# Performance work log

Hardware: AMD Instinct MI355X
Metric: run time of the kernel (lower is better)

Reference implementation:

```python
import jax, jax.numpy as jnp
import numpy as np

B, C, H, W = 8, 128, 96, 96
E = 8           # num_experts
K = 3           # active_experts
HID = 4 * C     # hidden dim of each expert (hidden_ratio=4)


def _conv1x1(x, w, b):
    # x: [B,C,H,W], w: [O,C], b: [O] -> [B,O,H,W]
    return jnp.einsum('bchw,oc->bohw', x, w) + b[None, :, None, None]


def setup_inputs() -> dict:
    key = jax.random.key(0)
    ks = jax.random.split(key, 12)
    s = lambda k, shape, fan_in: jax.random.normal(k, shape, jnp.float32) * (1.0 / np.sqrt(fan_in))
    return {
        'x':   jax.random.normal(ks[0], (B, C, H, W), jnp.float32),
        # shared expert: Conv2d(C->HID,1x1), GELU, Conv2d(HID->C,1x1)
        'sw1': s(ks[1], (HID, C), C),   'sb1': jnp.zeros((HID,), jnp.float32),
        'sw2': s(ks[2], (C, HID), HID), 'sb2': jnp.zeros((C,), jnp.float32),
        # router gate: Conv2d(C->E,1x1)
        'gw':  s(ks[3], (E, C), C),     'gb':  jnp.zeros((E,), jnp.float32),
        # stacked routed experts
        'ew1': s(ks[4], (E, HID, C), C),   'eb1': jnp.zeros((E, HID), jnp.float32),
        'ew2': s(ks[5], (E, C, HID), HID), 'eb2': jnp.zeros((E, C), jnp.float32),
    }


def reference(x, sw1, sb1, sw2, sb2, gw, gb, ew1, eb1, ew2, eb2):
    # shared expert (exact GELU, matching torch nn.GELU default)
    h_s = jax.nn.gelu(_conv1x1(x, sw1, sb1), approximate=False)
    shared_out = _conv1x1(h_s, sw2, sb2)

    # router: softmax over expert dim, top-k, renormalize
    logits = _conv1x1(x, gw, gb)                      # [B,E,H,W]
    scores = jax.nn.softmax(logits, axis=1)           # [B,E,H,W]
    s_last = jnp.transpose(scores, (0, 2, 3, 1))      # [B,H,W,E]
    topk_probs, topk_idx = jax.lax.top_k(s_last, K)   # [B,H,W,K]
    topk_probs = topk_probs / jnp.sum(topk_probs, axis=-1, keepdims=True)

    # expert_mask[b,e,h,w]: routing weight for expert e at location (scatter-equivalent)
    onehot = jax.nn.one_hot(topk_idx, E, dtype=x.dtype)        # [B,H,W,K,E]
    mask = jnp.einsum('bhwke,bhwk->behw', onehot, topk_probs)  # [B,E,H,W]

    # dense compute of all experts (faithful to original), masked combine
    h = jax.nn.gelu(jnp.einsum('bchw,eoc->beohw', x, ew1)
                    + eb1[None, :, :, None, None], approximate=False)  # [B,E,HID,H,W]
    y = jnp.einsum('beohw,eco->bechw', h, ew2) + eb2[None, :, :, None, None]
    moe_out = jnp.einsum('bechw,behw->bchw', y, mask)

    # load-balancing aux loss
    mean_prob = jnp.mean(scores, axis=(0, 2, 3))               # [E]
    mean_load = jnp.mean(jnp.sum(onehot, axis=3), axis=(0, 1, 2))  # [E]
    aux_loss = E * jnp.sum(mean_prob * mean_load)

    return (x + shared_out + moe_out, aux_loss)
```

## Files before the change

### kernel.cpp

```cpp
#include <hip/hip_runtime.h>


typedef __bf16 bf16x8 __attribute__((ext_vector_type(8)));
typedef __bf16 bf16x2 __attribute__((ext_vector_type(2)));
typedef unsigned short u16x8 __attribute__((ext_vector_type(8)));
typedef float f32x4 __attribute__((ext_vector_type(4)));

#define HWP 9216
#define NPIX 73728
#define LDX 136
#define LDH 136
#define LXP 68
#define MAXSLOTS 77312
#define MAXTILES 1208
#define NSH 16

__device__ __forceinline__ unsigned short f2bf(float f) {
    return __builtin_bit_cast(unsigned short, (__bf16)f);
}

__device__ __forceinline__ unsigned pk_bf16(float a, float b) {
    bf16x2 v; v[0] = (__bf16)a; v[1] = (__bf16)b;
    return __builtin_bit_cast(unsigned, v);
}

__device__ __forceinline__ float bf2f(unsigned short h) {
    return __uint_as_float((unsigned)h << 16);
}

__device__ __forceinline__ float fast_gelu(float x) {
    float x2 = x * x;
    float u = x * fmaf(0.0356774081f, x2, 0.7978845608f);
    float e = __builtin_amdgcn_exp2f(u * 2.8853900818f);
    float r = __builtin_amdgcn_rcpf(e + 1.0f);
    float t = fmaf(-2.0f, r, 1.0f);
    float s = 0.5f * x;
    return fmaf(s, t, s);
}

__device__ __forceinline__ f32x4 mfma16(u16x8 a, u16x8 b, f32x4 c) {
    return __builtin_amdgcn_mfma_f32_16x16x32_bf16(
        __builtin_bit_cast(bf16x8, a), __builtin_bit_cast(bf16x8, b), c, 0, 0, 0);
}

__global__ __launch_bounds__(256) void router_fused(
    const float* __restrict__ x, const float* __restrict__ gw,
    const float* __restrict__ gb,
    const float* __restrict__ sw1, const float* __restrict__ sw2,
    const float* __restrict__ ew1, const float* __restrict__ ew2,
    unsigned short* __restrict__ wbf,
    unsigned short* __restrict__ xT,
    int* __restrict__ pixmask, float* __restrict__ pixw3,
    int* __restrict__ pixaux,
    int* __restrict__ bincount, float* __restrict__ accum)
{
    __shared__ float gws[1024];
    __shared__ float xls[128 * LXP];
    __shared__ float part[4 * 64 * 8];

    const int tid = threadIdx.x;
    const int blk = blockIdx.x;
    const int shadow = blk & (NSH - 1);

    {
        int i = blk * 256 + tid;
        #pragma unroll
        for (int j = 0; j < 4; ++j) {
            float v;
            if (i < 65536) v = sw1[i];
            else if (i < 131072) v = sw2[i - 65536];
            else if (i < 655360) v = ew1[i - 131072];
            else v = ew2[i - 655360];
            wbf[i] = f2bf(v);
            i += 1152 * 256;
        }
    }

    for (int i = tid; i < 1024; i += 256) gws[i] = gw[i];

    const int b = blk / 144;
    const int p0 = (blk - b * 144) * 64;
    const float* xb = x + (size_t)b * 128 * HWP + p0;

    #pragma unroll
    for (int j = 0; j < 8; ++j) {
        int id4 = j * 256 + tid;
        int c = id4 >> 4;
        int g = id4 & 15;
        f32x4 v = *(const f32x4*)(xb + (size_t)c * HWP + g * 4);
        *(f32x4*)&xls[c * LXP + g * 4] = v;
    }
    __syncthreads();

    const int p = tid & 63, q = tid >> 6;
    {
        float lg[8];
        #pragma unroll
        for (int e = 0; e < 8; ++e) lg[e] = 0.f;
        #pragma unroll
        for (int k = 0; k < 32; ++k) {
            int c = q * 32 + k;
            float xv = xls[c * LXP + p];
            #pragma unroll
            for (int e = 0; e < 8; ++e) lg[e] = fmaf(xv, gws[e * 128 + c], lg[e]);
        }
        #pragma unroll
        for (int e = 0; e < 8; ++e) part[(q * 64 + p) * 8 + e] = lg[e];
    }
    __syncthreads();

    if (tid < 64) {
        const int gp = b * HWP + p0 + tid;
        float l2[8];
        #pragma unroll
        for (int e = 0; e < 8; ++e)
            l2[e] = gb[e] + part[tid * 8 + e] + part[(64 + tid) * 8 + e]
                  + part[(128 + tid) * 8 + e] + part[(192 + tid) * 8 + e];
        float mx = l2[0];
        #pragma unroll
        for (int e = 1; e < 8; ++e) mx = fmaxf(mx, l2[e]);
        float pr[8]; float s = 0.f;
        #pragma unroll
        for (int e = 0; e < 8; ++e) { pr[e] = __expf(l2[e] - mx); s += pr[e]; }
        float sinv = __builtin_amdgcn_rcpf(s);
        #pragma unroll
        for (int e = 0; e < 8; ++e) pr[e] *= sinv;

        unsigned chosen = 0; float topsum = 0.f;
        for (int k = 0; k < 3; ++k) {
            int best = 0; float bv = -1.f;
            #pragma unroll
            for (int e = 0; e < 8; ++e) {
                bool ok = !((chosen >> e) & 1u) && pr[e] > bv;
                bv = ok ? pr[e] : bv;
                best = ok ? e : best;
            }
            chosen |= 1u << best;
            topsum += bv;
        }
        float tinv = __builtin_amdgcn_rcpf(topsum);

        pixmask[gp] = (int)chosen;
        {
            int j = 0;
            #pragma unroll
            for (int e = 0; e < 8; ++e)
                if ((chosen >> e) & 1u) { pixw3[gp * 3 + j] = pr[e] * tinv; ++j; }
        }

        unsigned long long eq = ~0ull;
        #pragma unroll
        for (int bit = 0; bit < 8; ++bit) {
            unsigned long long bb = __ballot((chosen >> bit) & 1u);
            eq &= ((chosen >> bit) & 1u) ? bb : ~bb;
        }
        const unsigned long long lowmask = (tid == 0) ? 0ull : (~0ull >> (64 - tid));
        int rank = __popcll(eq & lowmask);
        int cnt = __popcll(eq);
        int leader = __ffsll((unsigned long long)eq) - 1;
        int off_val = 0;
        if (rank == 0) off_val = atomicAdd(&bincount[shadow * 256 + (int)chosen], cnt);
        int binoff = __shfl(off_val, leader);
        pixaux[gp] = binoff + rank;

        #pragma unroll
        for (int e = 0; e < 8; ++e) {
            float v = pr[e];
            float c2 = ((chosen >> e) & 1u) ? 1.f : 0.f;
            #pragma unroll
            for (int off = 32; off > 0; off >>= 1) {
                v += __shfl_down(v, off);
                c2 += __shfl_down(c2, off);
            }
            if (tid == 0) {
                atomicAdd(&accum[shadow * 16 + e], v);
                atomicAdd(&accum[shadow * 16 + 8 + e], c2);
            }
        }
    }

    {
        const int pp = tid >> 2, qq = tid & 3;
        unsigned short* dst = xT + ((size_t)(blk * 64 + pp)) * 128 + qq * 32;
        #pragma unroll
        for (int j = 0; j < 4; ++j) {
            const int c0 = qq * 32 + j * 8;
            uint4 wv;
            wv.x = pk_bf16(xls[(c0 + 0) * LXP + pp], xls[(c0 + 1) * LXP + pp]);
            wv.y = pk_bf16(xls[(c0 + 2) * LXP + pp], xls[(c0 + 3) * LXP + pp]);
            wv.z = pk_bf16(xls[(c0 + 4) * LXP + pp], xls[(c0 + 5) * LXP + pp]);
            wv.w = pk_bf16(xls[(c0 + 6) * LXP + pp], xls[(c0 + 7) * LXP + pp]);
            *(uint4*)(dst + j * 8) = wv;
        }
    }
}

__global__ __launch_bounds__(256) void fill_bins(
    const int* __restrict__ bincount, const int* __restrict__ pixmask,
    int* __restrict__ idx, int* __restrict__ pixaux,
    int* __restrict__ tileMask, int* __restrict__ tileBase,
    int* __restrict__ ntiles)
{
    __shared__ int spc[256], snt[256], bb[256];
    __shared__ int sbase[NSH][256];
    const int tid = threadIdx.x;
    int c = 0;
    #pragma unroll
    for (int s = 0; s < NSH; ++s) {
        sbase[s][tid] = c;
        c += bincount[s * 256 + tid];
    }
    const int nt = (c + 63) >> 6;
    const int pc = nt << 6;
    spc[tid] = pc; snt[tid] = nt;
    __syncthreads();
    #pragma unroll
    for (int off = 1; off < 256; off <<= 1) {
        int a = (tid >= off) ? spc[tid - off] : 0;
        int d = (tid >= off) ? snt[tid - off] : 0;
        __syncthreads();
        spc[tid] += a; snt[tid] += d;
        __syncthreads();
    }
    const int base = spc[tid] - pc;
    bb[tid] = base;
    if (blockIdx.x == 0) {
        const int tstart = snt[tid] - nt;
        for (int j = 0; j < nt; ++j) {
            tileMask[tstart + j] = tid;
            tileBase[tstart + j] = base + (j << 6);
        }
        if (tid == 255) ntiles[0] = snt[255];
    }
    __syncthreads();

    const int gp = blockIdx.x * 256 + tid;
    int mask = pixmask[gp];
    int shadow = (gp >> 6) & (NSH - 1);
    int slot = bb[mask] + sbase[shadow][mask] + pixaux[gp];
    idx[slot] = gp;
    pixaux[gp] = slot;
}

__global__ __launch_bounds__(256, 3) void moe_sparse(
    const unsigned short* __restrict__ xT, const int* __restrict__ idx,
    const float* __restrict__ pixw3,
    const int* __restrict__ tileMask, const int* __restrict__ tileBase,
    const int* __restrict__ ntiles,
    const unsigned short* __restrict__ wbf,
    const float* __restrict__ sb1, const float* __restrict__ sb2,
    const float* __restrict__ eb1, const float* __restrict__ eb2,
    unsigned short* __restrict__ outT)
{
    __shared__ unsigned short xs[64 * LDX];
    __shared__ unsigned short hs[64 * LDH];
    __shared__ float wls[64 * 4];

    const int t = blockIdx.x;
    if (t >= ntiles[0]) return;
    const int mask = tileMask[t];
    const int base = tileBase[t];
    const int tid = threadIdx.x;

    {
        const int p = tid >> 2, q = tid & 3;
        const int gp = idx[base + p];
        const unsigned short* src = xT + (size_t)gp * 128 + q * 32;
        unsigned short* dst = &xs[p * LDX + q * 32];
        #pragma unroll
        for (int j = 0; j < 4; ++j)
            *(u16x8*)(dst + j * 8) = *(const u16x8*)(src + j * 8);
        if (q == 0) {
            wls[p * 4 + 0] = pixw3[gp * 3 + 0];
            wls[p * 4 + 1] = pixw3[gp * 3 + 1];
            wls[p * 4 + 2] = pixw3[gp * 3 + 2];
        }
    }
    __syncthreads();

    int el[3];
    { int n = 0;
      #pragma unroll
      for (int e = 0; e < 8; ++e) if ((mask >> e) & 1) { if (n < 3) el[n] = e; ++n; } }

    const int wave = tid >> 6;
    const int lr = tid & 15;
    const int lq = (tid >> 4) & 3;

    const f32x4 vzero = {0.f, 0.f, 0.f, 0.f};
    f32x4 fin[2][4];
    #pragma unroll
    for (int t2 = 0; t2 < 2; ++t2)
        #pragma unroll
        for (int nt2 = 0; nt2 < 4; ++nt2) fin[t2][nt2] = vzero;

    for (int pass = 0; pass < 4; ++pass) {
        const unsigned short* w1; const unsigned short* w2;
        const float* b1;
        if (pass == 0) { w1 = wbf; b1 = sb1; w2 = wbf + 65536; }
        else {
            int e = el[pass - 1];
            w1 = wbf + 131072 + (size_t)e * (512 * 128);  b1 = eb1 + e * 512;
            w2 = wbf + 655360 + (size_t)e * (128 * 512);
        }

        float wtv[4];
        #pragma unroll
        for (int nt2 = 0; nt2 < 4; ++nt2)
            wtv[nt2] = (pass == 0) ? 1.0f : wls[(nt2 * 16 + lr) * 4 + (pass - 1)];

        for (int chunk = 0; chunk < 4; ++chunk) {
            u16x8 w1f[2][4];
            #pragma unroll
            for (int t2 = 0; t2 < 2; ++t2) {
                const int hid0 = chunk * 128 + wave * 32 + t2 * 16;
                const u16x8* wr = (const u16x8*)(w1 + (size_t)(hid0 + lr) * 128) + lq;
                #pragma unroll
                for (int ks = 0; ks < 4; ++ks) w1f[t2][ks] = wr[ks * 4];
            }
            f32x4 acc[2][4];
            #pragma unroll
            for (int t2 = 0; t2 < 2; ++t2)
                #pragma unroll
                for (int nt2 = 0; nt2 < 4; ++nt2) acc[t2][nt2] = vzero;
            __builtin_amdgcn_s_setprio(1);
            #pragma unroll
            for (int ks = 0; ks < 4; ++ks) {
                #pragma unroll
                for (int nt2 = 0; nt2 < 4; ++nt2) {
                    u16x8 xf = *(const u16x8*)&xs[(nt2 * 16 + lr) * LDX + ks * 32 + lq * 8];
                    acc[0][nt2] = mfma16(w1f[0][ks], xf, acc[0][nt2]);
                    acc[1][nt2] = mfma16(w1f[1][ks], xf, acc[1][nt2]);
                }
            }
            __builtin_amdgcn_s_setprio(0);

            u16x8 w2f[2][4];
            #pragma unroll
            for (int t2 = 0; t2 < 2; ++t2) {
                const int c0 = wave * 32 + t2 * 16;
                const u16x8* wr = (const u16x8*)(w2 + (size_t)(c0 + lr) * 512 + chunk * 128) + lq;
                #pragma unroll
                for (int ks = 0; ks < 4; ++ks) w2f[t2][ks] = wr[ks * 4];
            }

            #pragma unroll
            for (int t2 = 0; t2 < 2; ++t2) {
                const int hl = wave * 32 + t2 * 16 + lq * 4;
                const f32x4 b1v = *(const f32x4*)&b1[chunk * 128 + hl];
                #pragma unroll
                for (int nt2 = 0; nt2 < 4; ++nt2) {
                    float g0 = wtv[nt2] * fast_gelu(acc[t2][nt2][0] + b1v[0]);
                    float g1 = wtv[nt2] * fast_gelu(acc[t2][nt2][1] + b1v[1]);
                    float g2 = wtv[nt2] * fast_gelu(acc[t2][nt2][2] + b1v[2]);
                    float g3 = wtv[nt2] * fast_gelu(acc[t2][nt2][3] + b1v[3]);
                    uint2 wv = {pk_bf16(g0, g1), pk_bf16(g2, g3)};
                    *(uint2*)&hs[(nt2 * 16 + lr) * LDH + hl] = wv;
                }
            }
            __syncthreads();
            __builtin_amdgcn_s_setprio(1);
            #pragma unroll
            for (int ks = 0; ks < 4; ++ks) {
                #pragma unroll
                for (int nt2 = 0; nt2 < 4; ++nt2) {
                    u16x8 hb = *(const u16x8*)&hs[(nt2 * 16 + lr) * LDH + ks * 32 + lq * 8];
                    fin[0][nt2] = mfma16(w2f[0][ks], hb, fin[0][nt2]);
                    fin[1][nt2] = mfma16(w2f[1][ks], hb, fin[1][nt2]);
                }
            }
            __builtin_amdgcn_s_setprio(0);
            __syncthreads();
        }
    }

    #pragma unroll
    for (int t2 = 0; t2 < 2; ++t2) {
        const int cidx = wave * 32 + t2 * 16 + lq * 4;
        const f32x4 s2v = *(const f32x4*)&sb2[cidx];
        const f32x4 e0v = *(const f32x4*)&eb2[el[0] * 128 + cidx];
        const f32x4 e1v = *(const f32x4*)&eb2[el[1] * 128 + cidx];
        const f32x4 e2v = *(const f32x4*)&eb2[el[2] * 128 + cidx];
        #pragma unroll
        for (int nt2 = 0; nt2 < 4; ++nt2) {
            const float w0 = wls[(nt2 * 16 + lr) * 4 + 0];
            const float w1 = wls[(nt2 * 16 + lr) * 4 + 1];
            const float w2 = wls[(nt2 * 16 + lr) * 4 + 2];
            float o[4];
            #pragma unroll
            for (int r = 0; r < 4; ++r) {
                float bsum = s2v[r];
                bsum = fmaf(w0, e0v[r], bsum);
                bsum = fmaf(w1, e1v[r], bsum);
                bsum = fmaf(w2, e2v[r], bsum);
                o[r] = fin[t2][nt2][r] + bsum;
            }
            unsigned short* dst = outT + ((size_t)(base + nt2 * 16 + lr)) * 128
                                + wave * 32 + t2 * 16 + lq * 4;
            uint2 wv = {pk_bf16(o[0], o[1]), pk_bf16(o[2], o[3])};
            *(uint2*)dst = wv;
        }
    }
}

__global__ __launch_bounds__(256) void final_add(
    const float* __restrict__ x, const unsigned short* __restrict__ outT,
    const int* __restrict__ pixslot, const float* __restrict__ accum,
    float* __restrict__ out)
{
    if (blockIdx.x == 0 && threadIdx.x == 0) {
        float a16[16];
        #pragma unroll
        for (int i = 0; i < 16; ++i) {
            float s = 0.f;
            #pragma unroll
            for (int sh = 0; sh < NSH; ++sh) s += accum[sh * 16 + i];
            a16[i] = s;
        }
        float aux = 0.f;
        #pragma unroll
        for (int e = 0; e < 8; ++e) aux += a16[e] * a16[8 + e];
        out[9437184] = 8.0f * aux / ((float)NPIX * (float)NPIX);
    }
    __shared__ unsigned short ts[64 * 133];
    const int blk = blockIdx.x;
    const int b = blk / 144;
    const int p0 = (blk - b * 144) * 64;
    const int tid = threadIdx.x;
    {
        const int p = tid >> 2, q = tid & 3;
        const int slot = pixslot[blk * 64 + p];
        const unsigned short* src = outT + (size_t)slot * 128 + q * 32;
        unsigned short* dst = &ts[p * 133 + q * 32];
        #pragma unroll
        for (int j = 0; j < 4; ++j)
            *(u16x8*)(dst + j * 8) = *(const u16x8*)(src + j * 8);
    }
    __syncthreads();
    const int pl = tid & 63, cq = tid >> 6;
    const float* xb = x + (size_t)b * 128 * HWP + p0;
    float* ob = out + (size_t)b * 128 * HWP + p0;
    #pragma unroll
    for (int c0 = 0; c0 < 128; c0 += 4) {
        int c = c0 + cq;
        ob[(size_t)c * HWP + pl] = xb[(size_t)c * HWP + pl] + bf2f(ts[pl * 133 + c]);
    }
}

extern "C" void kernel_launch(void* const* d_in, const int* in_sizes, int n_in,
                              void* d_out, int out_size, void* d_ws, size_t ws_size,
                              hipStream_t stream)
{
    const float* x   = (const float*)d_in[0];
    const float* sw1 = (const float*)d_in[1];
    const float* sb1 = (const float*)d_in[2];
    const float* sw2 = (const float*)d_in[3];
    const float* sb2 = (const float*)d_in[4];
    const float* gw  = (const float*)d_in[5];
    const float* gb  = (const float*)d_in[6];
    const float* ew1 = (const float*)d_in[7];
    const float* eb1 = (const float*)d_in[8];
    const float* ew2 = (const float*)d_in[9];
    const float* eb2 = (const float*)d_in[10];
    float* out = (float*)d_out;
    char* ws = (char*)d_ws;

    const size_t o_wbf     = 0;
    const size_t o_xT      = 2359296;
    const size_t o_outT    = o_xT + 18874368;
    const size_t o_pixmask = o_outT + 19791872;
    const size_t o_pixw3   = o_pixmask + 294912;
    const size_t o_pixaux  = o_pixw3 + 884736;
    const size_t o_tmask   = o_pixaux + 294912;
    const size_t o_tbase   = o_tmask + 4864;
    const size_t o_idx     = o_tbase + 4864;
    const size_t o_cnt     = o_idx + 309248;
    const size_t o_ntiles  = o_cnt + 16384;
    const size_t o_accum   = o_ntiles + 16;
    const size_t MEMSET_SZ = 309248 + 16384 + 16 + 1024;

    unsigned short* wbf  = (unsigned short*)(ws + o_wbf);
    unsigned short* xT   = (unsigned short*)(ws + o_xT);
    unsigned short* outT = (unsigned short*)(ws + o_outT);
    int* pixmask  = (int*)(ws + o_pixmask);
    float* pixw3  = (float*)(ws + o_pixw3);
    int* pixaux   = (int*)(ws + o_pixaux);
    int* tmask    = (int*)(ws + o_tmask);
    int* tbase    = (int*)(ws + o_tbase);
    int* idx      = (int*)(ws + o_idx);
    int* bincount = (int*)(ws + o_cnt);
    int* ntiles   = (int*)(ws + o_ntiles);
    float* accum  = (float*)(ws + o_accum);

    (void)hipMemsetAsync(ws + o_idx, 0, MEMSET_SZ, stream);
    router_fused<<<1152, 256, 0, stream>>>(x, gw, gb, sw1, sw2, ew1, ew2, wbf,
                                           xT, pixmask, pixw3, pixaux, bincount, accum);
    fill_bins<<<288, 256, 0, stream>>>(bincount, pixmask, idx, pixaux,
                                       tmask, tbase, ntiles);
    moe_sparse<<<MAXTILES, 256, 0, stream>>>(xT, idx, pixw3, tmask, tbase, ntiles,
        wbf, sb1, sb2, eb1, eb2, outT);
    final_add<<<1152, 256, 0, stream>>>(x, outT, pixaux, accum, out);
}
```

Before: 321.6 us.

## Split moe_sparse work across 8 waves with 16-row slices per wave

Doubles the moe_sparse block from 4 to 8 waves. Each wave now owns 16 hidden/output rows instead of 32, which halves the per-wave accumulators and weight fragments. The x-tile load is spread over 512 threads. The aim is more resident waves to hide latency of global weight loads and LDS traffic, at the cost of each xs/hs fragment read being reused by only one MFMA instead of two, and more barrier participants.

```diff
diff --git a/kernel.cpp b/kernel.cpp
--- a/kernel.cpp
+++ b/kernel.cpp
@@ -242,7 +242,7 @@
     pixaux[gp] = slot;
 }
 
-__global__ __launch_bounds__(256, 3) void moe_sparse(
+__global__ __launch_bounds__(512, 6) void moe_sparse(
     const unsigned short* __restrict__ xT, const int* __restrict__ idx,
     const float* __restrict__ pixw3,
     const int* __restrict__ tileMask, const int* __restrict__ tileBase,
@@ -263,13 +263,12 @@
     const int tid = threadIdx.x;
 
     {
-        const int p = tid >> 2, q = tid & 3;
+        const int p = tid >> 3, q = tid & 7;
         const int gp = idx[base + p];
-        const unsigned short* src = xT + (size_t)gp * 128 + q * 32;
-        unsigned short* dst = &xs[p * LDX + q * 32];
-        #pragma unroll
-        for (int j = 0; j < 4; ++j)
-            *(u16x8*)(dst + j * 8) = *(const u16x8*)(src + j * 8);
+        const unsigned short* src = xT + (size_t)gp * 128 + q * 16;
+        unsigned short* dst = &xs[p * LDX + q * 16];
+        *(u16x8*)(dst + 0) = *(const u16x8*)(src + 0);
+        *(u16x8*)(dst + 8) = *(const u16x8*)(src + 8);
         if (q == 0) {
             wls[p * 4 + 0] = pixw3[gp * 3 + 0];
             wls[p * 4 + 1] = pixw3[gp * 3 + 1];
@@ -283,16 +282,14 @@
       #pragma unroll
       for (int e = 0; e < 8; ++e) if ((mask >> e) & 1) { if (n < 3) el[n] = e; ++n; } }
 
-    const int wave = tid >> 6;
+    const int w8 = tid >> 6;
     const int lr = tid & 15;
     const int lq = (tid >> 4) & 3;
 
     const f32x4 vzero = {0.f, 0.f, 0.f, 0.f};
-    f32x4 fin[2][4];
+    f32x4 fin[4];
     #pragma unroll
-    for (int t2 = 0; t2 < 2; ++t2)
-        #pragma unroll
-        for (int nt2 = 0; nt2 < 4; ++nt2) fin[t2][nt2] = vzero;
+    for (int nt2 = 0; nt2 < 4; ++nt2) fin[nt2] = vzero;
 
     for (int pass = 0; pass < 4; ++pass) {
         const unsigned short* w1; const unsigned short* w2;
@@ -310,50 +307,44 @@
             wtv[nt2] = (pass == 0) ? 1.0f : wls[(nt2 * 16 + lr) * 4 + (pass - 1)];
 
         for (int chunk = 0; chunk < 4; ++chunk) {
-            u16x8 w1f[2][4];
-            #pragma unroll
-            for (int t2 = 0; t2 < 2; ++t2) {
-                const int hid0 = chunk * 128 + wave * 32 + t2 * 16;
+            u16x8 w1f[4];
+            {
+                const int hid0 = chunk * 128 + w8 * 16;
                 const u16x8* wr = (const u16x8*)(w1 + (size_t)(hid0 + lr) * 128) + lq;
                 #pragma unroll
-                for (int ks = 0; ks < 4; ++ks) w1f[t2][ks] = wr[ks * 4];
-            }
-            f32x4 acc[2][4];
-            #pragma unroll
-            for (int t2 = 0; t2 < 2; ++t2)
-                #pragma unroll
-                for (int nt2 = 0; nt2 < 4; ++nt2) acc[t2][nt2] = vzero;
+                for (int ks = 0; ks < 4; ++ks) w1f[ks] = wr[ks * 4];
+            }
+            f32x4 acc[4];
+            #pragma unroll
+            for (int nt2 = 0; nt2 < 4; ++nt2) acc[nt2] = vzero;
             __builtin_amdgcn_s_setprio(1);
             #pragma unroll
             for (int ks = 0; ks < 4; ++ks) {
                 #pragma unroll
                 for (int nt2 = 0; nt2 < 4; ++nt2) {
                     u16x8 xf = *(const u16x8*)&xs[(nt2 * 16 + lr) * LDX + ks * 32 + lq * 8];
-                    acc[0][nt2] = mfma16(w1f[0][ks], xf, acc[0][nt2]);
-                    acc[1][nt2] = mfma16(w1f[1][ks], xf, acc[1][nt2]);
+                    acc[nt2] = mfma16(w1f[ks], xf, acc[nt2]);
                 }
             }
             __builtin_amdgcn_s_setprio(0);
 
-            u16x8 w2f[2][4];
-            #pragma unroll
-            for (int t2 = 0; t2 < 2; ++t2) {
-                const int c0 = wave * 32 + t2 * 16;
+            u16x8 w2f[4];
+            {
+                const int c0 = w8 * 16;
                 const u16x8* wr = (const u16x8*)(w2 + (size_t)(c0 + lr) * 512 + chunk * 128) + lq;
                 #pragma unroll
-                for (int ks = 0; ks < 4; ++ks) w2f[t2][ks] = wr[ks * 4];
-            }
-
-            #pragma unroll
-            for (int t2 = 0; t2 < 2; ++t2) {
-                const int hl = wave * 32 + t2 * 16 + lq * 4;
+                for (int ks = 0; ks < 4; ++ks) w2f[ks] = wr[ks * 4];
+            }
+
+            {
+                const int hl = w8 * 16 + lq * 4;
                 const f32x4 b1v = *(const f32x4*)&b1[chunk * 128 + hl];
                 #pragma unroll
                 for (int nt2 = 0; nt2 < 4; ++nt2) {
-                    float g0 = wtv[nt2] * fast_gelu(acc[t2][nt2][0] + b1v[0]);
-                    float g1 = wtv[nt2] * fast_gelu(acc[t2][nt2][1] + b1v[1]);
-                    float g2 = wtv[nt2] * fast_gelu(acc[t2][nt2][2] + b1v[2]);
-                    float g3 = wtv[nt2] * fast_gelu(acc[t2][nt2][3] + b1v[3]);
+                    float g0 = wtv[nt2] * fast_gelu(acc[nt2][0] + b1v[0]);
+                    float g1 = wtv[nt2] * fast_gelu(acc[nt2][1] + b1v[1]);
+                    float g2 = wtv[nt2] * fast_gelu(acc[nt2][2] + b1v[2]);
+                    float g3 = wtv[nt2] * fast_gelu(acc[nt2][3] + b1v[3]);
                     uint2 wv = {pk_bf16(g0, g1), pk_bf16(g2, g3)};
                     *(uint2*)&hs[(nt2 * 16 + lr) * LDH + hl] = wv;
                 }
@@ -365,8 +356,7 @@
                 #pragma unroll
                 for (int nt2 = 0; nt2 < 4; ++nt2) {
                     u16x8 hb = *(const u16x8*)&hs[(nt2 * 16 + lr) * LDH + ks * 32 + lq * 8];
-                    fin[0][nt2] = mfma16(w2f[0][ks], hb, fin[0][nt2]);
-                    fin[1][nt2] = mfma16(w2f[1][ks], hb, fin[1][nt2]);
+                    fin[nt2] = mfma16(w2f[ks], hb, fin[nt2]);
                 }
             }
             __builtin_amdgcn_s_setprio(0);
@@ -374,9 +364,8 @@
         }
     }
 
-    #pragma unroll
-    for (int t2 = 0; t2 < 2; ++t2) {
-        const int cidx = wave * 32 + t2 * 16 + lq * 4;
+    {
+        const int cidx = w8 * 16 + lq * 4;
         const f32x4 s2v = *(const f32x4*)&sb2[cidx];
         const f32x4 e0v = *(const f32x4*)&eb2[el[0] * 128 + cidx];
         const f32x4 e1v = *(const f32x4*)&eb2[el[1] * 128 + cidx];
@@ -393,10 +382,10 @@
                 bsum = fmaf(w0, e0v[r], bsum);
                 bsum = fmaf(w1, e1v[r], bsum);
                 bsum = fmaf(w2, e2v[r], bsum);
-                o[r] = fin[t2][nt2][r] + bsum;
+                o[r] = fin[nt2][r] + bsum;
             }
             unsigned short* dst = outT + ((size_t)(base + nt2 * 16 + lr)) * 128
-                                + wave * 32 + t2 * 16 + lq * 4;
+                                + w8 * 16 + lq * 4;
             uint2 wv = {pk_bf16(o[0], o[1]), pk_bf16(o[2], o[3])};
             *(uint2*)dst = wv;
         }
@@ -497,7 +486,7 @@
                                            xT, pixmask, pixw3, pixaux, bincount, accum);
     fill_bins<<<288, 256, 0, stream>>>(bincount, pixmask, idx, pixaux,
                                        tmask, tbase, ntiles);
-    moe_sparse<<<MAXTILES, 256, 0, stream>>>(xT, idx, pixw3, tmask, tbase, ntiles,
+    moe_sparse<<<MAXTILES, 512, 0, stream>>>(xT, idx, pixw3, tmask, tbase, ntiles,
         wbf, sb1, sb2, eb1, eb2, outT);
     final_add<<<1152, 256, 0, stream>>>(x, outT, pixaux, accum, out);
 }
```

Result: slower. 332.0 us (+3.2%).
